# Kernel tuning notes

Hardware: AMD Instinct MI355X
Metric: run time of the kernel (lower is better)

## Reference

```python
import jax, jax.numpy as jnp
import numpy as np

N_NODES = 100000
EMB_DIM = 64
HIDDEN = 8
OUT_DIM = 16
NUM_HEADS = 3
B = 1024
E_RAND = 3200000


def setup_inputs() -> dict:
    key = jax.random.key(0)
    ks = jax.random.split(key, 12)
    src = jax.random.randint(ks[0], (E_RAND,), 0, N_NODES, dtype=jnp.int32)
    dst = jax.random.randint(ks[1], (E_RAND,), 0, N_NODES, dtype=jnp.int32)
    loop = jnp.arange(N_NODES, dtype=jnp.int32)
    src = jnp.concatenate([src, loop])
    dst = jnp.concatenate([dst, loop])
    # multi-hot query indicator, ~50 items per query, guarantee >=1 item
    queries = (jax.random.uniform(ks[2], (B, N_NODES)) < 5e-4).astype(jnp.float32)
    queries = queries.at[:, 0].set(1.0)
    pos_items = jax.random.randint(ks[3], (B,), 0, N_NODES, dtype=jnp.int32)
    neg_items = jax.random.randint(ks[4], (B,), 0, N_NODES, dtype=jnp.int32)
    embedding = jax.random.normal(ks[5], (N_NODES, EMB_DIM), dtype=jnp.float32) * 0.1
    # GAT layer 1: NUM_HEADS heads, in=64 -> out=8 per head (concat)
    W1 = jax.random.normal(ks[6], (NUM_HEADS, EMB_DIM, HIDDEN), dtype=jnp.float32) * 0.1
    a1 = jax.random.normal(ks[7], (NUM_HEADS, 2 * HIDDEN), dtype=jnp.float32) * 0.1
    # GAT layer 2: 1 head, in=24 -> out=16
    W2 = jax.random.normal(ks[8], (NUM_HEADS * HIDDEN, OUT_DIM), dtype=jnp.float32) * 0.1
    a2 = jax.random.normal(ks[9], (2 * OUT_DIM,), dtype=jnp.float32) * 0.1
    return {"queries": queries, "pos_items": pos_items, "neg_items": neg_items,
            "embedding": embedding, "W1": W1, "a1": a1, "W2": W2, "a2": a2,
            "src": src, "dst": dst}


def gat_layer(h, W, a, src, dst, n_nodes):
    # h: [N, in], W: [H, in, o], a: [H, 2o]; returns [N, H, o]
    o = W.shape[-1]
    z = jnp.einsum('nd,hdo->nho', h, W)            # [N,H,o]
    zs, zd = z[src], z[dst]                         # [E,H,o]
    e = jax.nn.leaky_relu(
        jnp.einsum('eho,ho->eh', zs, a[:, :o]) +
        jnp.einsum('eho,ho->eh', zd, a[:, o:]), 0.01)  # [E,H]
    m = jax.ops.segment_max(e, dst, num_segments=n_nodes)       # [N,H]
    alpha = jnp.exp(e - m[dst])                                  # [E,H]
    denom = jax.ops.segment_sum(alpha, dst, num_segments=n_nodes)
    num = jax.ops.segment_sum(alpha[:, :, None] * zs, dst, num_segments=n_nodes)
    return num / denom[:, :, None]


def gat_forward(embedding, W1, a1, W2, a2, src, dst):
    n = embedding.shape[0]
    h1 = gat_layer(embedding, W1, a1, src, dst, n)       # [N,H,hid]
    h1 = jax.nn.elu(h1.reshape(n, -1))                   # [N,H*hid]
    h2 = gat_layer(h1, W2[None], a2[None], src, dst, n)  # [N,1,out]
    return h2[:, 0]                                      # [N,out]


def reference(queries, pos_items, neg_items, embedding, W1, a1, W2, a2, src, dst):
    item_embeds = gat_forward(embedding, W1, a1, W2, a2, src, dst)  # [N,16]
    item_cnt = jnp.sum(queries, axis=1)                              # [B]
    query_embeds = jnp.matmul(queries, item_embeds) / item_cnt[:, None]
    pos_embed = item_embeds[pos_items]
    neg_embed = item_embeds[neg_items]
    return (query_embeds, pos_embed, neg_embed)
```

## Files before the change

kernel.cpp:

```cpp
#include <hip/hip_runtime.h>

#define NH 3
#define HID 8
#define C1 24
#define C2 16
#define BSH 6
#define BNODES 64
#define NBMAX 1600
#define SCAP 3072
#define PCHUNK 16384

__global__ __launch_bounds__(256) void k_z1(
    const float* __restrict__ emb, const float* __restrict__ W1g,
    const float* __restrict__ a1g, float* __restrict__ z1,
    float4* __restrict__ f1s, float4* __restrict__ f1d, int N) {
    __shared__ float sW[NH * 64 * HID];
    __shared__ float sa[NH * 2 * HID];
    for (int i = threadIdx.x; i < NH * 64 * HID; i += blockDim.x) sW[i] = W1g[i];
    for (int i = threadIdx.x; i < NH * 2 * HID; i += blockDim.x) sa[i] = a1g[i];
    __syncthreads();
    int n = blockIdx.x * blockDim.x + threadIdx.x;
    if (n >= N) return;
    float e[64];
    const float4* ep = (const float4*)(emb + (size_t)n * 64);
#pragma unroll
    for (int i = 0; i < 16; ++i) {
        float4 v = ep[i];
        e[4*i+0] = v.x; e[4*i+1] = v.y; e[4*i+2] = v.z; e[4*i+3] = v.w;
    }
    float z[C1];
#pragma unroll
    for (int c = 0; c < C1; ++c) z[c] = 0.f;
    for (int d = 0; d < 64; ++d) {
        float ed = e[d];
#pragma unroll
        for (int h = 0; h < NH; ++h) {
            const float4* wp = (const float4*)&sW[(h * 64 + d) * HID];
            float4 w0 = wp[0], w1 = wp[1];
            z[h*HID+0] += ed * w0.x; z[h*HID+1] += ed * w0.y;
            z[h*HID+2] += ed * w0.z; z[h*HID+3] += ed * w0.w;
            z[h*HID+4] += ed * w1.x; z[h*HID+5] += ed * w1.y;
            z[h*HID+6] += ed * w1.z; z[h*HID+7] += ed * w1.w;
        }
    }
    float4* zp = (float4*)(z1 + (size_t)n * C1);
#pragma unroll
    for (int i = 0; i < 6; ++i)
        zp[i] = make_float4(z[4*i], z[4*i+1], z[4*i+2], z[4*i+3]);
    float fs[NH], fd[NH];
#pragma unroll
    for (int h = 0; h < NH; ++h) {
        float s = 0.f, dsum = 0.f;
#pragma unroll
        for (int o = 0; o < HID; ++o) {
            s    += z[h*HID+o] * sa[h*2*HID + o];
            dsum += z[h*HID+o] * sa[h*2*HID + HID + o];
        }
        fs[h] = s; fd[h] = dsum;
    }
    f1s[n] = make_float4(fs[0], fs[1], fs[2], 0.f);
    f1d[n] = make_float4(fd[0], fd[1], fd[2], 0.f);
}

__global__ void k_zero(int* __restrict__ p, int n) {
    int i = blockIdx.x * blockDim.x + threadIdx.x;
    if (i < n) p[i] = 0;
}

__global__ __launch_bounds__(256) void k_count(const int* __restrict__ dst,
                                               int* __restrict__ bcnt, int E, int NB) {
    __shared__ int lh[NBMAX];
    for (int i = threadIdx.x; i < NB; i += 256) lh[i] = 0;
    __syncthreads();
    int base = blockIdx.x * PCHUNK;
    int end = base + PCHUNK; if (end > E) end = E;
    for (int i = base + threadIdx.x; i < end; i += 256)
        atomicAdd(&lh[dst[i] >> BSH], 1);
    __syncthreads();
    for (int i = threadIdx.x; i < NB; i += 256)
        if (lh[i]) atomicAdd(&bcnt[i], lh[i]);
}

__global__ __launch_bounds__(256) void k_bscan(const int* __restrict__ bcnt,
                                               int* __restrict__ boff,
                                               int* __restrict__ bcur,
                                               int* __restrict__ rowptr,
                                               int NB, int N, int E) {
    __shared__ int sd[256];
    int tid = threadIdx.x;
    int v[8]; int tsum = 0;
#pragma unroll
    for (int i = 0; i < 8; ++i) {
        int g = tid * 8 + i;
        v[i] = (g < NB) ? bcnt[g] : 0;
        tsum += v[i];
    }
    sd[tid] = tsum; __syncthreads();
    for (int off = 1; off < 256; off <<= 1) {
        int t = (tid >= off) ? sd[tid - off] : 0;
        __syncthreads();
        sd[tid] += t;
        __syncthreads();
    }
    int pref = sd[tid] - tsum;
#pragma unroll
    for (int i = 0; i < 8; ++i) {
        int g = tid * 8 + i;
        if (g < NB) { boff[g] = pref; bcur[g] = pref; pref += v[i]; }
    }
    if (tid == 255) boff[NB] = pref;
    if (tid == 0) rowptr[N] = E;
}

__global__ __launch_bounds__(256) void k_part(const int* __restrict__ src,
                                              const int* __restrict__ dst,
                                              int* __restrict__ bcur,
                                              int* __restrict__ bedges, int E, int NB) {
    __shared__ int lh[NBMAX];
    __shared__ int lbase[NBMAX];
    for (int i = threadIdx.x; i < NB; i += 256) lh[i] = 0;
    __syncthreads();
    int base = blockIdx.x * PCHUNK;
    int end = base + PCHUNK; if (end > E) end = E;
    for (int i = base + threadIdx.x; i < end; i += 256)
        atomicAdd(&lh[dst[i] >> BSH], 1);
    __syncthreads();
    for (int i = threadIdx.x; i < NB; i += 256) {
        int c = lh[i];
        lbase[i] = c ? atomicAdd(&bcur[i], c) : 0;
        lh[i] = 0;
    }
    __syncthreads();
    for (int i = base + threadIdx.x; i < end; i += 256) {
        int d = dst[i];
        int b = d >> BSH;
        int p = lbase[b] + atomicAdd(&lh[b], 1);
        bedges[p] = src[i] | ((d & (BNODES - 1)) << 17);
    }
}

__global__ __launch_bounds__(256) void k_gat1s(
    const int* __restrict__ boff, int* __restrict__ bedges,
    const float* __restrict__ z1, const float4* __restrict__ f1s,
    const float4* __restrict__ f1d,
    const float* __restrict__ W2g, const float* __restrict__ a2g,
    float* __restrict__ z2, float* __restrict__ f2s, float* __restrict__ f2d,
    int* __restrict__ rowptr, int N) {
    __shared__ int ssrc[SCAP];
    __shared__ int scnt[BNODES];
    __shared__ int sstart[BNODES + 1];
    __shared__ int scur[BNODES];
    __shared__ float sW2[C1 * C2];
    __shared__ float sa2[2 * C2];
    int tid = threadIdx.x;
    int b = blockIdx.x;
    int beg = boff[b], cnt = boff[b + 1] - beg;
    if (tid < BNODES) scnt[tid] = 0;
    for (int i = tid; i < C1 * C2; i += 256) sW2[i] = W2g[i];
    if (tid < 2 * C2) sa2[tid] = a2g[tid];
    __syncthreads();
    for (int i = tid; i < cnt; i += 256)
        atomicAdd(&scnt[bedges[beg + i] >> 17], 1);
    __syncthreads();
    if (tid < 64) {
        int v = scnt[tid];
        int x = v;
        for (int d = 1; d < 64; d <<= 1) {
            int t = __shfl_up(x, d, 64);
            if (tid >= d) x += t;
        }
        sstart[tid] = x - v;
        scur[tid] = x - v;
        if (tid == 63) sstart[64] = x;
    }
    __syncthreads();
    for (int i = tid; i < cnt; i += 256) {
        int pk = bedges[beg + i];
        int p = atomicAdd(&scur[pk >> 17], 1);
        ssrc[p] = pk & 0x1FFFF;
    }
    __syncthreads();
    for (int i = tid; i < cnt; i += 256) bedges[beg + i] = ssrc[i];
    int n0 = b << BSH;
    if (tid < BNODES) {
        int n = n0 + tid;
        if (n < N) rowptr[n] = beg + sstart[tid];
    }
    int nl = tid >> 2, l4 = tid & 3;
    int n = n0 + nl;
    int s0 = sstart[nl], s1 = sstart[nl + 1];
    float4 fdv = (n < N) ? f1d[n] : make_float4(0.f, 0.f, 0.f, 0.f);
    float acc[C1];
#pragma unroll
    for (int c = 0; c < C1; ++c) acc[c] = 0.f;
    float den0 = 0.f, den1 = 0.f, den2 = 0.f;
    for (int i = s0 + l4; i < s1; i += 4) {
        int s = ssrc[i];
        float4 fsv = f1s[s];
        float e0 = fsv.x + fdv.x, e1 = fsv.y + fdv.y, e2 = fsv.z + fdv.z;
        e0 = e0 > 0.f ? e0 : 0.01f * e0;
        e1 = e1 > 0.f ? e1 : 0.01f * e1;
        e2 = e2 > 0.f ? e2 : 0.01f * e2;
        float a0 = __expf(e0), a1 = __expf(e1), a2v = __expf(e2);
        den0 += a0; den1 += a1; den2 += a2v;
        const float4* zp = (const float4*)(z1 + (size_t)s * C1);
        float4 q0 = zp[0], q1 = zp[1], q2 = zp[2], q3 = zp[3], q4 = zp[4], q5 = zp[5];
        acc[0]  += a0 * q0.x; acc[1]  += a0 * q0.y; acc[2]  += a0 * q0.z; acc[3]  += a0 * q0.w;
        acc[4]  += a0 * q1.x; acc[5]  += a0 * q1.y; acc[6]  += a0 * q1.z; acc[7]  += a0 * q1.w;
        acc[8]  += a1 * q2.x; acc[9]  += a1 * q2.y; acc[10] += a1 * q2.z; acc[11] += a1 * q2.w;
        acc[12] += a1 * q3.x; acc[13] += a1 * q3.y; acc[14] += a1 * q3.z; acc[15] += a1 * q3.w;
        acc[16] += a2v * q4.x; acc[17] += a2v * q4.y; acc[18] += a2v * q4.z; acc[19] += a2v * q4.w;
        acc[20] += a2v * q5.x; acc[21] += a2v * q5.y; acc[22] += a2v * q5.z; acc[23] += a2v * q5.w;
    }
#pragma unroll
    for (int c = 0; c < C1; ++c) {
        acc[c] += __shfl_xor(acc[c], 1, 64);
        acc[c] += __shfl_xor(acc[c], 2, 64);
    }
    den0 += __shfl_xor(den0, 1, 64); den0 += __shfl_xor(den0, 2, 64);
    den1 += __shfl_xor(den1, 1, 64); den1 += __shfl_xor(den1, 2, 64);
    den2 += __shfl_xor(den2, 1, 64); den2 += __shfl_xor(den2, 2, 64);
    if (l4 == 0 && n < N) {
        float h1v[C1];
        float inv0 = 1.f / den0, inv1 = 1.f / den1, inv2 = 1.f / den2;
#pragma unroll
        for (int o = 0; o < HID; ++o) {
            float v0 = acc[o] * inv0;
            float v1 = acc[HID + o] * inv1;
            float v2 = acc[2 * HID + o] * inv2;
            h1v[o]           = v0 > 0.f ? v0 : (__expf(v0) - 1.f);
            h1v[HID + o]     = v1 > 0.f ? v1 : (__expf(v1) - 1.f);
            h1v[2 * HID + o] = v2 > 0.f ? v2 : (__expf(v2) - 1.f);
        }
        float zz[C2];
#pragma unroll
        for (int k = 0; k < C2; ++k) zz[k] = 0.f;
        for (int c = 0; c < C1; ++c) {
            float hv = h1v[c];
#pragma unroll
            for (int k = 0; k < C2; ++k) zz[k] += hv * sW2[c * C2 + k];
        }
        float fs = 0.f, fdd = 0.f;
#pragma unroll
        for (int k = 0; k < C2; ++k) {
            fs  += zz[k] * sa2[k];
            fdd += zz[k] * sa2[C2 + k];
        }
        float4* zo = (float4*)(z2 + (size_t)n * C2);
#pragma unroll
        for (int i = 0; i < 4; ++i)
            zo[i] = make_float4(zz[4*i], zz[4*i+1], zz[4*i+2], zz[4*i+3]);
        f2s[n] = fs;
        f2d[n] = fdd;
    }
}

__global__ __launch_bounds__(256) void k_gat2(
    const int* __restrict__ rowptr, const int* __restrict__ csr,
    const float* __restrict__ z2, const float* __restrict__ f2s,
    const float* __restrict__ f2d, float* __restrict__ item, int N) {
    int t = blockIdx.x * blockDim.x + threadIdx.x;
    int n = t >> 2, l4 = t & 3;
    if (n >= N) return;
    int beg = rowptr[n], end = rowptr[n + 1];
    float fdv = f2d[n];
    float acc[C2];
#pragma unroll
    for (int k = 0; k < C2; ++k) acc[k] = 0.f;
    float den = 0.f;
    for (int i = beg + l4; i < end; i += 4) {
        int s = csr[i];
        float e = f2s[s] + fdv;
        e = e > 0.f ? e : 0.01f * e;
        float a = __expf(e);
        den += a;
        const float4* zp = (const float4*)(z2 + (size_t)s * C2);
        float4 q0 = zp[0], q1 = zp[1], q2 = zp[2], q3 = zp[3];
        acc[0]  += a * q0.x; acc[1]  += a * q0.y; acc[2]  += a * q0.z; acc[3]  += a * q0.w;
        acc[4]  += a * q1.x; acc[5]  += a * q1.y; acc[6]  += a * q1.z; acc[7]  += a * q1.w;
        acc[8]  += a * q2.x; acc[9]  += a * q2.y; acc[10] += a * q2.z; acc[11] += a * q2.w;
        acc[12] += a * q3.x; acc[13] += a * q3.y; acc[14] += a * q3.z; acc[15] += a * q3.w;
    }
#pragma unroll
    for (int k = 0; k < C2; ++k) {
        acc[k] += __shfl_xor(acc[k], 1, 64);
        acc[k] += __shfl_xor(acc[k], 2, 64);
    }
    den += __shfl_xor(den, 1, 64);
    den += __shfl_xor(den, 2, 64);
    if (l4 == 0) {
        float inv = 1.f / den;
        float4* io = (float4*)(item + (size_t)n * C2);
#pragma unroll
        for (int i = 0; i < 4; ++i)
            io[i] = make_float4(acc[4*i]*inv, acc[4*i+1]*inv, acc[4*i+2]*inv, acc[4*i+3]*inv);
    }
}

__global__ __launch_bounds__(256) void k_query(
    const float* __restrict__ queries, const float* __restrict__ item,
    float* __restrict__ out, int N) {
    int b = blockIdx.x;
    const float4* qrow = (const float4*)(queries + (size_t)b * N);
    int n4 = N >> 2;
    float acc[C2];
#pragma unroll
    for (int k = 0; k < C2; ++k) acc[k] = 0.f;
    float cnt = 0.f;
    for (int i = threadIdx.x; i < n4; i += 256) {
        float4 v = qrow[i];
        int j = i * 4;
        float vv[4] = {v.x, v.y, v.z, v.w};
#pragma unroll
        for (int c = 0; c < 4; ++c) {
            if (vv[c] != 0.f) {
                cnt += vv[c];
                const float4* rp = (const float4*)(item + (size_t)(j + c) * C2);
                float4 r0 = rp[0], r1 = rp[1], r2 = rp[2], r3 = rp[3];
                acc[0]  += vv[c]*r0.x; acc[1]  += vv[c]*r0.y; acc[2]  += vv[c]*r0.z; acc[3]  += vv[c]*r0.w;
                acc[4]  += vv[c]*r1.x; acc[5]  += vv[c]*r1.y; acc[6]  += vv[c]*r1.z; acc[7]  += vv[c]*r1.w;
                acc[8]  += vv[c]*r2.x; acc[9]  += vv[c]*r2.y; acc[10] += vv[c]*r2.z; acc[11] += vv[c]*r2.w;
                acc[12] += vv[c]*r3.x; acc[13] += vv[c]*r3.y; acc[14] += vv[c]*r3.z; acc[15] += vv[c]*r3.w;
            }
        }
    }
    int rem = N & 3;
    if ((int)threadIdx.x < rem) {
        int j = n4 * 4 + threadIdx.x;
        float qv = queries[(size_t)b * N + j];
        if (qv != 0.f) {
            cnt += qv;
#pragma unroll
            for (int k = 0; k < C2; ++k) acc[k] += qv * item[(size_t)j * C2 + k];
        }
    }
    __shared__ float red[4][C2 + 1];
    int lane = threadIdx.x & 63, wid = threadIdx.x >> 6;
#pragma unroll
    for (int k = 0; k < C2; ++k)
        for (int off = 32; off; off >>= 1) acc[k] += __shfl_down(acc[k], off, 64);
    for (int off = 32; off; off >>= 1) cnt += __shfl_down(cnt, off, 64);
    if (lane == 0) {
#pragma unroll
        for (int k = 0; k < C2; ++k) red[wid][k] = acc[k];
        red[wid][C2] = cnt;
    }
    __syncthreads();
    if (threadIdx.x < C2 + 1) {
        float s = red[0][threadIdx.x] + red[1][threadIdx.x] +
                  red[2][threadIdx.x] + red[3][threadIdx.x];
        red[0][threadIdx.x] = s;
    }
    __syncthreads();
    if (threadIdx.x < C2)
        out[(size_t)b * C2 + threadIdx.x] = red[0][threadIdx.x] / red[0][C2];
}

__global__ void k_posneg(const int* __restrict__ pos, const int* __restrict__ neg,
                         const float* __restrict__ item, float* __restrict__ out, int B) {
    int idx = blockIdx.x * blockDim.x + threadIdx.x;
    int total = 2 * B * C2;
    if (idx >= total) return;
    int which = idx / (B * C2);
    int r = idx - which * B * C2;
    int b = r / C2, k = r - b * C2;
    int node = which ? neg[b] : pos[b];
    out[(size_t)B * C2 + idx] = item[(size_t)node * C2 + k];
}

extern "C" void kernel_launch(void* const* d_in, const int* in_sizes, int n_in,
                              void* d_out, int out_size, void* d_ws, size_t ws_size,
                              hipStream_t stream) {
    const float* queries = (const float*)d_in[0];
    const int*   pos     = (const int*)d_in[1];
    const int*   neg     = (const int*)d_in[2];
    const float* emb     = (const float*)d_in[3];
    const float* W1      = (const float*)d_in[4];
    const float* a1      = (const float*)d_in[5];
    const float* W2      = (const float*)d_in[6];
    const float* a2      = (const float*)d_in[7];
    const int*   src     = (const int*)d_in[8];
    const int*   dst     = (const int*)d_in[9];

    int B = in_sizes[1];
    int N = in_sizes[3] / 64;
    int E = in_sizes[8];
    float* out = (float*)d_out;

    int NB = (N + BNODES - 1) >> BSH;

    char* w = (char*)d_ws;
    auto alloc = [&](size_t bytes) -> char* {
        char* p = w;
        w += (bytes + 255) & ~(size_t)255;
        return p;
    };
    float*  z1     = (float*)alloc(sizeof(float) * (size_t)N * C1);
    float4* f1s    = (float4*)alloc(sizeof(float4) * (size_t)N);
    float4* f1d    = (float4*)alloc(sizeof(float4) * (size_t)N);
    float*  z2     = (float*)alloc(sizeof(float) * (size_t)N * C2);
    float*  f2s    = (float*)alloc(sizeof(float) * (size_t)N);
    float*  f2d    = (float*)alloc(sizeof(float) * (size_t)N);
    float*  item   = (float*)alloc(sizeof(float) * (size_t)N * C2);
    int*    bcnt   = (int*)alloc(sizeof(int) * (size_t)NB);
    int*    boff   = (int*)alloc(sizeof(int) * (size_t)(NB + 1));
    int*    bcur   = (int*)alloc(sizeof(int) * (size_t)NB);
    int*    rowptr = (int*)alloc(sizeof(int) * (size_t)(N + 1));
    int*    bedges = (int*)alloc(sizeof(int) * (size_t)E);

    int nblkN = (N + 255) / 256;
    int nPart = (E + PCHUNK - 1) / PCHUNK;

    k_z1<<<nblkN, 256, 0, stream>>>(emb, W1, a1, z1, f1s, f1d, N);
    k_zero<<<(NB + 255) / 256, 256, 0, stream>>>(bcnt, NB);
    k_count<<<nPart, 256, 0, stream>>>(dst, bcnt, E, NB);
    k_bscan<<<1, 256, 0, stream>>>(bcnt, boff, bcur, rowptr, NB, N, E);
    k_part<<<nPart, 256, 0, stream>>>(src, dst, bcur, bedges, E, NB);
    k_gat1s<<<NB, 256, 0, stream>>>(boff, bedges, z1, f1s, f1d, W2, a2,
                                    z2, f2s, f2d, rowptr, N);
    k_gat2<<<(N * 4 + 255) / 256, 256, 0, stream>>>(rowptr, bedges, z2, f2s, f2d, item, N);
    k_query<<<B, 256, 0, stream>>>(queries, item, out, N);
    k_posneg<<<(2 * B * C2 + 255) / 256, 256, 0, stream>>>(pos, neg, item, out, B);
}
```

Before: 880.8 us.

## Pack source attention scalars with z1 rows and use 8 lanes per node

Merges the per-node source attention logits and the 24-wide z1 features into a single 128-byte padded row, so each edge gather in the layer-1 aggregation reads one contiguous cache line instead of two separate arrays. Buckets shrink from 64 to 32 nodes and each destination node now gets 8 lanes instead of 4 in both GAT aggregation kernels, adding a third shuffle-reduction step. This trades extra padding bytes and more blocks for better per-edge parallelism and fewer scattered loads. The rowptr write also drops its n<N bounds check.

```diff
diff --git a/kernel.cpp b/kernel.cpp
--- a/kernel.cpp
+++ b/kernel.cpp
@@ -4,16 +4,17 @@
 #define HID 8
 #define C1 24
 #define C2 16
-#define BSH 6
-#define BNODES 64
-#define NBMAX 1600
-#define SCAP 3072
+#define BSH 5
+#define BNODES 32
+#define NBMAX 3200
+#define SCAP 1792
 #define PCHUNK 16384
+#define AZS 32
 
 __global__ __launch_bounds__(256) void k_z1(
     const float* __restrict__ emb, const float* __restrict__ W1g,
-    const float* __restrict__ a1g, float* __restrict__ z1,
-    float4* __restrict__ f1s, float4* __restrict__ f1d, int N) {
+    const float* __restrict__ a1g, float* __restrict__ az1,
+    float4* __restrict__ f1d, int N) {
     __shared__ float sW[NH * 64 * HID];
     __shared__ float sa[NH * 2 * HID];
     for (int i = threadIdx.x; i < NH * 64 * HID; i += blockDim.x) sW[i] = W1g[i];
@@ -43,10 +44,6 @@
             z[h*HID+6] += ed * w1.z; z[h*HID+7] += ed * w1.w;
         }
     }
-    float4* zp = (float4*)(z1 + (size_t)n * C1);
-#pragma unroll
-    for (int i = 0; i < 6; ++i)
-        zp[i] = make_float4(z[4*i], z[4*i+1], z[4*i+2], z[4*i+3]);
     float fs[NH], fd[NH];
 #pragma unroll
     for (int h = 0; h < NH; ++h) {
@@ -58,7 +55,12 @@
         }
         fs[h] = s; fd[h] = dsum;
     }
-    f1s[n] = make_float4(fs[0], fs[1], fs[2], 0.f);
+    float4* zp = (float4*)(az1 + (size_t)n * AZS);
+    zp[0] = make_float4(fs[0], fs[1], fs[2], 0.f);
+#pragma unroll
+    for (int i = 0; i < 6; ++i)
+        zp[1 + i] = make_float4(z[4*i], z[4*i+1], z[4*i+2], z[4*i+3]);
+    zp[7] = make_float4(0.f, 0.f, 0.f, 0.f);
     f1d[n] = make_float4(fd[0], fd[1], fd[2], 0.f);
 }
 
@@ -81,6 +83,7 @@
         if (lh[i]) atomicAdd(&bcnt[i], lh[i]);
 }
 
+#define SCANK 13
 __global__ __launch_bounds__(256) void k_bscan(const int* __restrict__ bcnt,
                                                int* __restrict__ boff,
                                                int* __restrict__ bcur,
@@ -88,10 +91,10 @@
                                                int NB, int N, int E) {
     __shared__ int sd[256];
     int tid = threadIdx.x;
-    int v[8]; int tsum = 0;
-#pragma unroll
-    for (int i = 0; i < 8; ++i) {
-        int g = tid * 8 + i;
+    int v[SCANK]; int tsum = 0;
+#pragma unroll
+    for (int i = 0; i < SCANK; ++i) {
+        int g = tid * SCANK + i;
         v[i] = (g < NB) ? bcnt[g] : 0;
         tsum += v[i];
     }
@@ -104,8 +107,8 @@
     }
     int pref = sd[tid] - tsum;
 #pragma unroll
-    for (int i = 0; i < 8; ++i) {
-        int g = tid * 8 + i;
+    for (int i = 0; i < SCANK; ++i) {
+        int g = tid * SCANK + i;
         if (g < NB) { boff[g] = pref; bcur[g] = pref; pref += v[i]; }
     }
     if (tid == 255) boff[NB] = pref;
@@ -139,10 +142,9 @@
     }
 }
 
-__global__ __launch_bounds__(256) void k_gat1s(
+__global__ __launch_bounds__(256) void k_gat1(
     const int* __restrict__ boff, int* __restrict__ bedges,
-    const float* __restrict__ z1, const float4* __restrict__ f1s,
-    const float4* __restrict__ f1d,
+    const float* __restrict__ az1, const float4* __restrict__ f1d,
     const float* __restrict__ W2g, const float* __restrict__ a2g,
     float* __restrict__ z2, float* __restrict__ f2s, float* __restrict__ f2d,
     int* __restrict__ rowptr, int N) {
@@ -162,16 +164,16 @@
     for (int i = tid; i < cnt; i += 256)
         atomicAdd(&scnt[bedges[beg + i] >> 17], 1);
     __syncthreads();
-    if (tid < 64) {
+    if (tid < BNODES) {
         int v = scnt[tid];
         int x = v;
-        for (int d = 1; d < 64; d <<= 1) {
+        for (int d = 1; d < BNODES; d <<= 1) {
             int t = __shfl_up(x, d, 64);
             if (tid >= d) x += t;
         }
         sstart[tid] = x - v;
         scur[tid] = x - v;
-        if (tid == 63) sstart[64] = x;
+        if (tid == BNODES - 1) sstart[BNODES] = x;
     }
     __syncthreads();
     for (int i = tid; i < cnt; i += 256) {
@@ -182,11 +184,8 @@
     __syncthreads();
     for (int i = tid; i < cnt; i += 256) bedges[beg + i] = ssrc[i];
     int n0 = b << BSH;
-    if (tid < BNODES) {
-        int n = n0 + tid;
-        if (n < N) rowptr[n] = beg + sstart[tid];
-    }
-    int nl = tid >> 2, l4 = tid & 3;
+    if (tid < BNODES) rowptr[n0 + tid] = beg + sstart[tid];
+    int nl = tid >> 3, l8 = tid & 7;
     int n = n0 + nl;
     int s0 = sstart[nl], s1 = sstart[nl + 1];
     float4 fdv = (n < N) ? f1d[n] : make_float4(0.f, 0.f, 0.f, 0.f);
@@ -194,33 +193,34 @@
 #pragma unroll
     for (int c = 0; c < C1; ++c) acc[c] = 0.f;
     float den0 = 0.f, den1 = 0.f, den2 = 0.f;
-    for (int i = s0 + l4; i < s1; i += 4) {
+    for (int i = s0 + l8; i < s1; i += 8) {
         int s = ssrc[i];
-        float4 fsv = f1s[s];
-        float e0 = fsv.x + fdv.x, e1 = fsv.y + fdv.y, e2 = fsv.z + fdv.z;
+        const float4* zp = (const float4*)(az1 + ((size_t)s << 5));
+        float4 q0 = zp[0], q1 = zp[1], q2 = zp[2], q3 = zp[3],
+               q4 = zp[4], q5 = zp[5], q6 = zp[6];
+        float e0 = q0.x + fdv.x, e1 = q0.y + fdv.y, e2 = q0.z + fdv.z;
         e0 = e0 > 0.f ? e0 : 0.01f * e0;
         e1 = e1 > 0.f ? e1 : 0.01f * e1;
         e2 = e2 > 0.f ? e2 : 0.01f * e2;
         float a0 = __expf(e0), a1 = __expf(e1), a2v = __expf(e2);
         den0 += a0; den1 += a1; den2 += a2v;
-        const float4* zp = (const float4*)(z1 + (size_t)s * C1);
-        float4 q0 = zp[0], q1 = zp[1], q2 = zp[2], q3 = zp[3], q4 = zp[4], q5 = zp[5];
-        acc[0]  += a0 * q0.x; acc[1]  += a0 * q0.y; acc[2]  += a0 * q0.z; acc[3]  += a0 * q0.w;
-        acc[4]  += a0 * q1.x; acc[5]  += a0 * q1.y; acc[6]  += a0 * q1.z; acc[7]  += a0 * q1.w;
-        acc[8]  += a1 * q2.x; acc[9]  += a1 * q2.y; acc[10] += a1 * q2.z; acc[11] += a1 * q2.w;
-        acc[12] += a1 * q3.x; acc[13] += a1 * q3.y; acc[14] += a1 * q3.z; acc[15] += a1 * q3.w;
-        acc[16] += a2v * q4.x; acc[17] += a2v * q4.y; acc[18] += a2v * q4.z; acc[19] += a2v * q4.w;
-        acc[20] += a2v * q5.x; acc[21] += a2v * q5.y; acc[22] += a2v * q5.z; acc[23] += a2v * q5.w;
+        acc[0]  += a0 * q1.x; acc[1]  += a0 * q1.y; acc[2]  += a0 * q1.z; acc[3]  += a0 * q1.w;
+        acc[4]  += a0 * q2.x; acc[5]  += a0 * q2.y; acc[6]  += a0 * q2.z; acc[7]  += a0 * q2.w;
+        acc[8]  += a1 * q3.x; acc[9]  += a1 * q3.y; acc[10] += a1 * q3.z; acc[11] += a1 * q3.w;
+        acc[12] += a1 * q4.x; acc[13] += a1 * q4.y; acc[14] += a1 * q4.z; acc[15] += a1 * q4.w;
+        acc[16] += a2v * q5.x; acc[17] += a2v * q5.y; acc[18] += a2v * q5.z; acc[19] += a2v * q5.w;
+        acc[20] += a2v * q6.x; acc[21] += a2v * q6.y; acc[22] += a2v * q6.z; acc[23] += a2v * q6.w;
     }
 #pragma unroll
     for (int c = 0; c < C1; ++c) {
         acc[c] += __shfl_xor(acc[c], 1, 64);
         acc[c] += __shfl_xor(acc[c], 2, 64);
-    }
-    den0 += __shfl_xor(den0, 1, 64); den0 += __shfl_xor(den0, 2, 64);
-    den1 += __shfl_xor(den1, 1, 64); den1 += __shfl_xor(den1, 2, 64);
-    den2 += __shfl_xor(den2, 1, 64); den2 += __shfl_xor(den2, 2, 64);
-    if (l4 == 0 && n < N) {
+        acc[c] += __shfl_xor(acc[c], 4, 64);
+    }
+    den0 += __shfl_xor(den0, 1, 64); den0 += __shfl_xor(den0, 2, 64); den0 += __shfl_xor(den0, 4, 64);
+    den1 += __shfl_xor(den1, 1, 64); den1 += __shfl_xor(den1, 2, 64); den1 += __shfl_xor(den1, 4, 64);
+    den2 += __shfl_xor(den2, 1, 64); den2 += __shfl_xor(den2, 2, 64); den2 += __shfl_xor(den2, 4, 64);
+    if (l8 == 0 && n < N) {
         float h1v[C1];
         float inv0 = 1.f / den0, inv1 = 1.f / den1, inv2 = 1.f / den2;
 #pragma unroll
@@ -260,7 +260,7 @@
     const float* __restrict__ z2, const float* __restrict__ f2s,
     const float* __restrict__ f2d, float* __restrict__ item, int N) {
     int t = blockIdx.x * blockDim.x + threadIdx.x;
-    int n = t >> 2, l4 = t & 3;
+    int n = t >> 3, l8 = t & 7;
     if (n >= N) return;
     int beg = rowptr[n], end = rowptr[n + 1];
     float fdv = f2d[n];
@@ -268,7 +268,7 @@
 #pragma unroll
     for (int k = 0; k < C2; ++k) acc[k] = 0.f;
     float den = 0.f;
-    for (int i = beg + l4; i < end; i += 4) {
+    for (int i = beg + l8; i < end; i += 8) {
         int s = csr[i];
         float e = f2s[s] + fdv;
         e = e > 0.f ? e : 0.01f * e;
@@ -285,10 +285,12 @@
     for (int k = 0; k < C2; ++k) {
         acc[k] += __shfl_xor(acc[k], 1, 64);
         acc[k] += __shfl_xor(acc[k], 2, 64);
+        acc[k] += __shfl_xor(acc[k], 4, 64);
     }
     den += __shfl_xor(den, 1, 64);
     den += __shfl_xor(den, 2, 64);
-    if (l4 == 0) {
+    den += __shfl_xor(den, 4, 64);
+    if (l8 == 0) {
         float inv = 1.f / den;
         float4* io = (float4*)(item + (size_t)n * C2);
 #pragma unroll
@@ -395,8 +397,7 @@
         w += (bytes + 255) & ~(size_t)255;
         return p;
     };
-    float*  z1     = (float*)alloc(sizeof(float) * (size_t)N * C1);
-    float4* f1s    = (float4*)alloc(sizeof(float4) * (size_t)N);
+    float*  az1    = (float*)alloc(sizeof(float) * (size_t)N * AZS);
     float4* f1d    = (float4*)alloc(sizeof(float4) * (size_t)N);
     float*  z2     = (float*)alloc(sizeof(float) * (size_t)N * C2);
     float*  f2s    = (float*)alloc(sizeof(float) * (size_t)N);
@@ -411,14 +412,14 @@
     int nblkN = (N + 255) / 256;
     int nPart = (E + PCHUNK - 1) / PCHUNK;
 
-    k_z1<<<nblkN, 256, 0, stream>>>(emb, W1, a1, z1, f1s, f1d, N);
+    k_z1<<<nblkN, 256, 0, stream>>>(emb, W1, a1, az1, f1d, N);
     k_zero<<<(NB + 255) / 256, 256, 0, stream>>>(bcnt, NB);
     k_count<<<nPart, 256, 0, stream>>>(dst, bcnt, E, NB);
     k_bscan<<<1, 256, 0, stream>>>(bcnt, boff, bcur, rowptr, NB, N, E);
     k_part<<<nPart, 256, 0, stream>>>(src, dst, bcur, bedges, E, NB);
-    k_gat1s<<<NB, 256, 0, stream>>>(boff, bedges, z1, f1s, f1d, W2, a2,
-                                    z2, f2s, f2d, rowptr, N);
-    k_gat2<<<(N * 4 + 255) / 256, 256, 0, stream>>>(rowptr, bedges, z2, f2s, f2d, item, N);
+    k_gat1<<<NB, 256, 0, stream>>>(boff, bedges, az1, f1d, W2, a2,
+                                   z2, f2s, f2d, rowptr, N);
+    k_gat2<<<(N * 8 + 255) / 256, 256, 0, stream>>>(rowptr, bedges, z2, f2s, f2d, item, N);
     k_query<<<B, 256, 0, stream>>>(queries, item, out, N);
     k_posneg<<<(2 * B * C2 + 255) / 256, 256, 0, stream>>>(pos, neg, item, out, B);
 }
```

After: 857.0 us. 2.7% less time.
